# Performance work log

Measured on AMD Instinct MI355X. Metric: run time of the kernel, lower is better.

The kernel has to match this reference:

```python
import jax, jax.numpy as jnp
import numpy as np

B, CIN, COUT, H, W, K, S = 32, 16, 32, 14, 14, 5, 2


def _conv(x, w, stride, groups=1):
    # x: [N, Cin_g*groups, H, W], w: [Cout, Cin_g, K, K], VALID padding, no bias
    return jax.lax.conv_general_dilated(
        x, w, (stride, stride), 'VALID',
        dimension_numbers=('NCHW', 'OIHW', 'NCHW'),
        feature_group_count=groups)


def setup_inputs() -> dict:
    key = jax.random.key(0)
    k1, k2, k3 = jax.random.split(key, 3)
    u = jax.random.normal(k1, (B, CIN, H, W), jnp.float32)
    C = jax.random.normal(k2, (B, CIN, H, W, H, W), jnp.float32)
    # per-output-channel single-channel kernels, as in Conv2d(1,1,K) list
    w = jax.random.normal(k3, (COUT, 1, K, K), jnp.float32) * (1.0 / K)
    return {"u": u, "C": C, "w": w}


def reference(u, C, w):
    b, cin, h, wd = u.shape
    cout = w.shape[0]
    # ---- mean path: conv each input channel with every kernel, sum over Cin ----
    m = _conv(u.reshape(b * cin, 1, h, wd), w, S)          # [b*cin, cout, OH, OW]
    oh, ow = m.shape[2], m.shape[3]
    out_mean = m.reshape(b, cin, cout, oh, ow).sum(axis=1)  # [b, cout, OH, OW]

    # ---- covariance path: apply the same conv to both spatial index pairs ----
    # conv over original dims (4,5)
    t = _conv(C.reshape(b * cin * h * wd, 1, h, wd), w, S)  # [b*cin*h*w, cout, OH, OW]
    t = t.reshape(b, cin, h, wd, cout, oh, ow)
    # bring original dims (2,3) to conv position; keep kernel index as channel
    t = t.transpose(0, 1, 5, 6, 4, 2, 3)                    # [b, cin, OH, OW, cout, h, w]
    t = t.reshape(b * cin * oh * ow, cout, h, wd)
    # grouped conv: channel i convolved with kernel i (second application)
    t = _conv(t, w, S, groups=cout)                         # [b*cin*OH*OW, cout, OH, OW]
    t = t.reshape(b, cin, oh, ow, cout, oh, ow)             # [b,c,oh45,ow45,i,oh23,ow23]
    # torch output layout: [b, i, oh23, ow23, oh45, ow45], summed over cin
    out_cov = t.transpose(0, 4, 5, 6, 2, 3, 1).sum(axis=-1)
    return (out_mean, out_cov)
```

## Files before the change

### kernel.cpp

```cpp
#include <hip/hip_runtime.h>


#define NB   32
#define NCIN 16
#define NCO  32
#define HH   14
#define OO   5
#define HW   196
#define T1_PER_BI 4900

__device__ float g_T1[NB * NCO * T1_PER_BI];

__global__ __launch_bounds__(448) void k1_reduce_conv(const float* __restrict__ C,
                                                      const float* __restrict__ w) {
  const int blk = blockIdx.x;
  const int b   = blk / HH;
  const int h1  = blk % HH;
  const int tid = threadIdx.x;

  __shared__ float wl[NCO * 25];
  __shared__ float cs[14 * 224];
  __shared__ float t1s[448 * 25];

  for (int t = tid; t < NCO * 25; t += 448) wl[t] = w[t];

  const float4* C4 = (const float4*)C;
  const int base4 = ((b * NCIN) * HH + h1) * 686;
  for (int j4 = tid; j4 < 686; j4 += 448) {
    float4 acc = make_float4(0.f, 0.f, 0.f, 0.f);
    #pragma unroll
    for (int c = 0; c < NCIN; ++c) {
      float4 v = C4[base4 + c * 9604 + j4];
      acc.x += v.x; acc.y += v.y; acc.z += v.z; acc.w += v.w;
    }
    const float vv[4] = {acc.x, acc.y, acc.z, acc.w};
    const int j = j4 * 4;
    #pragma unroll
    for (int e = 0; e < 4; ++e) {
      const int jj = j + e;
      const int w1 = jj / 196, rem = jj % 196;
      const int h2 = rem / 14, w2 = rem % 14;
      cs[w1 * 224 + h2 * 16 + w2] = vv[e];
    }
  }
  __syncthreads();

  const int i  = tid & 31;
  const int w1 = tid >> 5;
  float wr[25];
  #pragma unroll
  for (int t = 0; t < 25; ++t) wr[t] = wl[i * 25 + t];

  float acc[25];
  #pragma unroll
  for (int t = 0; t < 25; ++t) acc[t] = 0.f;

  #pragma unroll
  for (int r = 0; r < 5; ++r) {
    #pragma unroll
    for (int cc = 0; cc < 5; ++cc) {
      const int row = 2 * r + cc;
      const float4* rp = (const float4*)(cs + w1 * 224 + row * 16);
      float4 x0 = rp[0], x1 = rp[1], x2 = rp[2], x3 = rp[3];
      const float col[16] = {x0.x, x0.y, x0.z, x0.w,
                             x1.x, x1.y, x1.z, x1.w,
                             x2.x, x2.y, x2.z, x2.w,
                             x3.x, x3.y, x3.z, x3.w};
      #pragma unroll
      for (int s = 0; s < 5; ++s) {
        #pragma unroll
        for (int d = 0; d < 5; ++d)
          acc[r * 5 + s] += wr[cc * 5 + d] * col[2 * s + d];
      }
    }
  }

  #pragma unroll
  for (int t = 0; t < 25; ++t) t1s[i * 350 + w1 * 25 + t] = acc[t];
  __syncthreads();

  const size_t gbase = (size_t)b * NCO * T1_PER_BI + (size_t)h1 * 350;
  for (int idx = tid; idx < 11200; idx += 448) {
    const int i2 = idx / 350, rem = idx % 350;
    g_T1[gbase + (size_t)i2 * T1_PER_BI + rem] = t1s[idx];
  }
}

__global__ __launch_bounds__(128) void k2_out(const float* __restrict__ u,
                                              const float* __restrict__ w,
                                              float* __restrict__ out) {
  const int blk = blockIdx.x;
  const int tid = threadIdx.x;

  if (blk < NB * NCO) {
    __shared__ float sl[T1_PER_BI];
    const float4* src = (const float4*)(g_T1 + (size_t)blk * T1_PER_BI);
    float4* sl4 = (float4*)sl;
    for (int j = tid; j < 1225; j += 128) sl4[j] = src[j];

    const int i = blk & 31;
    float wr[25];
    #pragma unroll
    for (int t = 0; t < 25; ++t) wr[t] = w[i * 25 + t];
    __syncthreads();

    for (int o = tid; o < 625; o += 128) {
      const int p  = o / 125;
      const int q  = (o / 25) % 5;
      const int rs = o % 25;
      float acc = 0.f;
      #pragma unroll
      for (int a = 0; a < 5; ++a) {
        #pragma unroll
        for (int bb = 0; bb < 5; ++bb)
          acc += wr[a * 5 + bb] * sl[((2 * p + a) * 14 + (2 * q + bb)) * 25 + rs];
      }
      out[25600 + blk * 625 + o] = acc;
    }
  } else {
    const int b = blk - NB * NCO;
    __shared__ float us[HW];
    for (int j = tid; j < HW; j += 128) {
      float acc = 0.f;
      #pragma unroll
      for (int c = 0; c < NCIN; ++c) acc += u[(b * NCIN + c) * HW + j];
      us[j] = acc;
    }
    __syncthreads();
    for (int o = tid; o < NCO * 25; o += 128) {
      const int i = o / 25;
      const int p = (o / 5) % 5;
      const int q = o % 5;
      float acc = 0.f;
      #pragma unroll
      for (int a = 0; a < 5; ++a) {
        #pragma unroll
        for (int bb = 0; bb < 5; ++bb)
          acc += w[i * 25 + a * 5 + bb] * us[(2 * p + a) * 14 + 2 * q + bb];
      }
      out[b * 800 + o] = acc;
    }
  }
}

extern "C" void kernel_launch(void* const* d_in, const int* in_sizes, int n_in,
                              void* d_out, int out_size, void* d_ws, size_t ws_size,
                              hipStream_t stream) {
  const float* u = (const float*)d_in[0];
  const float* C = (const float*)d_in[1];
  const float* w = (const float*)d_in[2];
  float* out = (float*)d_out;

  hipLaunchKernelGGL(k1_reduce_conv, dim3(NB * HH), dim3(448), 0, stream, C, w);
  hipLaunchKernelGGL(k2_out, dim3(NB * NCO + NB), dim3(128), 0, stream, u, w, out);
}
```

Measured before the change: 135.6 us.

## Skip unused h1 row, pad T1 slabs, and swizzle blocks for XCD locality

The stride-2, kernel-5 second conv only reads input rows 0..12, so the first kernel now skips h1=13 (and w1=13), shrinking the intermediate T1 from 14x14 to 13x13 per (b,i). Each slab is padded to 328 floats so the global store is float4-vectorized, and shared memory is merged into a single reused buffer. Block indices in both kernels are remapped so that a batch's blocks land on the same XCD (blockIdx & 7), aiming at L2 locality between producer and consumer. k2 block size also goes from 128 to 256 threads.

```diff
diff --git a/kernel.cpp b/kernel.cpp
--- a/kernel.cpp
+++ b/kernel.cpp
@@ -5,22 +5,23 @@
 #define NCIN 16
 #define NCO  32
 #define HH   14
-#define OO   5
-#define HW   196
-#define T1_PER_BI 4900
+#define OH13 13
+#define SLAB 328
+#define T1_PER_BI  4264
+#define T1_PER_BI4 1066
 
 __device__ float g_T1[NB * NCO * T1_PER_BI];
 
 __global__ __launch_bounds__(448) void k1_reduce_conv(const float* __restrict__ C,
                                                       const float* __restrict__ w) {
-  const int blk = blockIdx.x;
-  const int b   = blk / HH;
-  const int h1  = blk % HH;
-  const int tid = threadIdx.x;
+  const int xcd  = blockIdx.x & 7;
+  const int slot = blockIdx.x >> 3;
+  const int b    = xcd + 8 * (slot / OH13);
+  const int h1   = slot % OH13;
+  const int tid  = threadIdx.x;
 
   __shared__ float wl[NCO * 25];
-  __shared__ float cs[14 * 224];
-  __shared__ float t1s[448 * 25];
+  __shared__ __align__(16) float buf[NCO * SLAB];
 
   for (int t = tid; t < NCO * 25; t += 448) wl[t] = w[t];
 
@@ -34,13 +35,14 @@
       acc.x += v.x; acc.y += v.y; acc.z += v.z; acc.w += v.w;
     }
     const float vv[4] = {acc.x, acc.y, acc.z, acc.w};
-    const int j = j4 * 4;
+    const int j    = j4 * 4;
+    const int w1   = j / 196;
+    const int rem0 = j - w1 * 196;
     #pragma unroll
     for (int e = 0; e < 4; ++e) {
-      const int jj = j + e;
-      const int w1 = jj / 196, rem = jj % 196;
-      const int h2 = rem / 14, w2 = rem % 14;
-      cs[w1 * 224 + h2 * 16 + w2] = vv[e];
+      const int rem = rem0 + e;
+      const int h2 = rem / 14, w2 = rem - h2 * 14;
+      buf[w1 * 224 + h2 * 16 + w2] = vv[e];
     }
   }
   __syncthreads();
@@ -55,56 +57,73 @@
   #pragma unroll
   for (int t = 0; t < 25; ++t) acc[t] = 0.f;
 
-  #pragma unroll
-  for (int r = 0; r < 5; ++r) {
+  if (w1 < OH13) {
     #pragma unroll
-    for (int cc = 0; cc < 5; ++cc) {
-      const int row = 2 * r + cc;
-      const float4* rp = (const float4*)(cs + w1 * 224 + row * 16);
-      float4 x0 = rp[0], x1 = rp[1], x2 = rp[2], x3 = rp[3];
-      const float col[16] = {x0.x, x0.y, x0.z, x0.w,
-                             x1.x, x1.y, x1.z, x1.w,
-                             x2.x, x2.y, x2.z, x2.w,
-                             x3.x, x3.y, x3.z, x3.w};
+    for (int r = 0; r < 5; ++r) {
       #pragma unroll
-      for (int s = 0; s < 5; ++s) {
+      for (int cc = 0; cc < 5; ++cc) {
+        const int row = 2 * r + cc;
+        const float4* rp = (const float4*)(buf + w1 * 224 + row * 16);
+        float4 x0 = rp[0], x1 = rp[1], x2 = rp[2], x3 = rp[3];
+        const float col[16] = {x0.x, x0.y, x0.z, x0.w,
+                               x1.x, x1.y, x1.z, x1.w,
+                               x2.x, x2.y, x2.z, x2.w,
+                               x3.x, x3.y, x3.z, x3.w};
         #pragma unroll
-        for (int d = 0; d < 5; ++d)
-          acc[r * 5 + s] += wr[cc * 5 + d] * col[2 * s + d];
+        for (int s = 0; s < 5; ++s) {
+          #pragma unroll
+          for (int d = 0; d < 5; ++d)
+            acc[r * 5 + s] += wr[cc * 5 + d] * col[2 * s + d];
+        }
       }
     }
   }
-
-  #pragma unroll
-  for (int t = 0; t < 25; ++t) t1s[i * 350 + w1 * 25 + t] = acc[t];
   __syncthreads();
 
-  const size_t gbase = (size_t)b * NCO * T1_PER_BI + (size_t)h1 * 350;
-  for (int idx = tid; idx < 11200; idx += 448) {
-    const int i2 = idx / 350, rem = idx % 350;
-    g_T1[gbase + (size_t)i2 * T1_PER_BI + rem] = t1s[idx];
+  if (w1 < OH13) {
+    #pragma unroll
+    for (int t = 0; t < 25; ++t) buf[i * SLAB + w1 * 25 + t] = acc[t];
+  } else {
+    buf[i * SLAB + 325] = 0.f;
+    buf[i * SLAB + 326] = 0.f;
+    buf[i * SLAB + 327] = 0.f;
+  }
+  __syncthreads();
+
+  const float4* t1s4 = (const float4*)buf;
+  float4* G4 = (float4*)g_T1;
+  const int gbase4 = (b * NCO) * T1_PER_BI4 + h1 * 82;
+  for (int idx4 = tid; idx4 < NCO * 82; idx4 += 448) {
+    const int i2  = idx4 / 82;
+    const int rem = idx4 - i2 * 82;
+    G4[gbase4 + i2 * T1_PER_BI4 + rem] = t1s4[idx4];
   }
 }
 
-__global__ __launch_bounds__(128) void k2_out(const float* __restrict__ u,
+__global__ __launch_bounds__(256) void k2_out(const float* __restrict__ u,
                                               const float* __restrict__ w,
                                               float* __restrict__ out) {
   const int blk = blockIdx.x;
   const int tid = threadIdx.x;
 
   if (blk < NB * NCO) {
-    __shared__ float sl[T1_PER_BI];
-    const float4* src = (const float4*)(g_T1 + (size_t)blk * T1_PER_BI);
+    const int xcd  = blk & 7;
+    const int slot = blk >> 3;
+    const int b    = xcd + 8 * (slot >> 5);
+    const int i    = slot & 31;
+    const int bi   = b * NCO + i;
+
+    __shared__ __align__(16) float sl[T1_PER_BI];
+    const float4* src = (const float4*)(g_T1 + (size_t)bi * T1_PER_BI);
     float4* sl4 = (float4*)sl;
-    for (int j = tid; j < 1225; j += 128) sl4[j] = src[j];
+    for (int j = tid; j < T1_PER_BI4; j += 256) sl4[j] = src[j];
 
-    const int i = blk & 31;
     float wr[25];
     #pragma unroll
     for (int t = 0; t < 25; ++t) wr[t] = w[i * 25 + t];
     __syncthreads();
 
-    for (int o = tid; o < 625; o += 128) {
+    for (int o = tid; o < 625; o += 256) {
       const int p  = o / 125;
       const int q  = (o / 25) % 5;
       const int rs = o % 25;
@@ -113,21 +132,21 @@
       for (int a = 0; a < 5; ++a) {
         #pragma unroll
         for (int bb = 0; bb < 5; ++bb)
-          acc += wr[a * 5 + bb] * sl[((2 * p + a) * 14 + (2 * q + bb)) * 25 + rs];
+          acc += wr[a * 5 + bb] * sl[(2 * p + a) * SLAB + (2 * q + bb) * 25 + rs];
       }
-      out[25600 + blk * 625 + o] = acc;
+      out[25600 + bi * 625 + o] = acc;
     }
   } else {
     const int b = blk - NB * NCO;
-    __shared__ float us[HW];
-    for (int j = tid; j < HW; j += 128) {
+    __shared__ float us[196];
+    for (int j = tid; j < 196; j += 256) {
       float acc = 0.f;
       #pragma unroll
-      for (int c = 0; c < NCIN; ++c) acc += u[(b * NCIN + c) * HW + j];
+      for (int c = 0; c < NCIN; ++c) acc += u[(b * NCIN + c) * 196 + j];
       us[j] = acc;
     }
     __syncthreads();
-    for (int o = tid; o < NCO * 25; o += 128) {
+    for (int o = tid; o < NCO * 25; o += 256) {
       const int i = o / 25;
       const int p = (o / 5) % 5;
       const int q = o % 5;
@@ -151,6 +170,6 @@
   const float* w = (const float*)d_in[2];
   float* out = (float*)d_out;
 
-  hipLaunchKernelGGL(k1_reduce_conv, dim3(NB * HH), dim3(448), 0, stream, C, w);
-  hipLaunchKernelGGL(k2_out, dim3(NB * NCO + NB), dim3(128), 0, stream, u, w, out);
+  hipLaunchKernelGGL(k1_reduce_conv, dim3(8 * 52), dim3(448), 0, stream, C, w);
+  hipLaunchKernelGGL(k2_out, dim3(NB * NCO + NB), dim3(256), 0, stream, u, w, out);
 }
```

New measurement: 126.1 us. -7.0%, faster.
